# Kernel tuning notes

Measured on AMD Instinct MI355X. Metric: run time of the kernel, lower is better.

## Reference

```python
import jax, jax.numpy as jnp
import numpy as np

NC, NG, NP = 8192, 4096, 140
FD, D, L = 512, 256, 2
E_OBS, E_COEXP, E_PPI, E_SYM = 300000, 200000, 10000, 20000
EPS = 1e-5


def layer_norm(x, g, b):
    mu = jnp.mean(x, -1, keepdims=True)
    v = jnp.mean((x - mu) ** 2, -1, keepdims=True)
    return (x - mu) * jax.lax.rsqrt(v + EPS) * g + b


def sage(h_src, h_dst, src, dst, w, Ws, Wn, b, n_dst):
    # DGL SAGEConv (mean aggregator, edge-weighted): mean over incoming
    # weighted messages, then fc_self(h_dst) + fc_neigh(neigh) + bias.
    m = h_src[src] * w[:, None]                                  # [E, D]
    neigh = jax.ops.segment_sum(m, dst, num_segments=n_dst)      # [n_dst, D]
    deg = jax.ops.segment_sum(jnp.ones_like(w), dst, num_segments=n_dst)
    neigh = neigh / jnp.maximum(deg, 1.0)[:, None]
    return h_dst @ Ws + neigh @ Wn + b


def setup_inputs() -> dict:
    key = jax.random.key(0)
    ks = iter(jax.random.split(key, 64))
    def n(*s):
        return jax.random.normal(next(ks), s, jnp.float32) * 0.02
    def u(e):
        return jax.random.uniform(next(ks), (e,), jnp.float32)
    def ri(e, hi):
        return jax.random.randint(next(ks), (e,), 0, hi, jnp.int32)
    return dict(
        cell_feat=jax.random.normal(next(ks), (NC, FD), jnp.float32),
        gene_feat=jax.random.normal(next(ks), (NG, FD), jnp.float32),
        pro_idx=jnp.arange(NP, dtype=jnp.int32),
        obs_src=ri(E_OBS, NG), obs_dst=ri(E_OBS, NC), obs_w=u(E_OBS),
        rev_obs_src=ri(E_OBS, NC), rev_obs_dst=ri(E_OBS, NG), rev_obs_w=u(E_OBS),
        symbol_src=ri(E_SYM, NG), symbol_dst=ri(E_SYM, NP), symbol_w=u(E_SYM),
        rev_symbol_src=ri(E_SYM, NP), rev_symbol_dst=ri(E_SYM, NG), rev_symbol_w=u(E_SYM),
        coexp_src=ri(E_COEXP, NG), coexp_dst=ri(E_COEXP, NG), coexp_w=u(E_COEXP),
        ppi_src=ri(E_PPI, NP), ppi_dst=ri(E_PPI, NP), ppi_w=u(E_PPI),
        W_emb_cell=n(FD, D), b_emb_cell=jnp.zeros((D,), jnp.float32),
        W_emb_gene=n(FD, D), b_emb_gene=jnp.zeros((D,), jnp.float32),
        emb_pro=n(NP, D),
        W_mlpcell=n(L, D, D), b_mlpcell=jnp.zeros((L, D), jnp.float32),
        W_sage_self=n(L, 6, D, D), W_sage_neigh=n(L, 6, D, D),
        b_sage=jnp.zeros((L, 6, D), jnp.float32),
        ln1_g=jnp.ones((L, 3, D), jnp.float32), ln1_b=jnp.zeros((L, 3, D), jnp.float32),
        ln2_g=jnp.ones((L, 3, D), jnp.float32), ln2_b=jnp.zeros((L, 3, D), jnp.float32),
        W_last=n(3 * D, NP), b_last=jnp.zeros((NP,), jnp.float32),
    )


def reference(cell_feat, gene_feat, pro_idx,
              obs_src, obs_dst, obs_w,
              rev_obs_src, rev_obs_dst, rev_obs_w,
              symbol_src, symbol_dst, symbol_w,
              rev_symbol_src, rev_symbol_dst, rev_symbol_w,
              coexp_src, coexp_dst, coexp_w,
              ppi_src, ppi_dst, ppi_w,
              W_emb_cell, b_emb_cell, W_emb_gene, b_emb_gene, emb_pro,
              W_mlpcell, b_mlpcell, W_sage_self, W_sage_neigh, b_sage,
              ln1_g, ln1_b, ln2_g, ln2_b, W_last, b_last):
    act = jax.nn.selu
    hc = cell_feat @ W_emb_cell + b_emb_cell      # emb_cell
    hg = gene_feat @ W_emb_gene + b_emb_gene      # emb_gene
    hp = emb_pro[pro_idx]                         # nn.Embedding path
    nc, ng, npn = hc.shape[0], hg.shape[0], hp.shape[0]
    hist = [hc]
    for l in range(W_mlpcell.shape[0]):
        Ws, Wn, bs = W_sage_self[l], W_sage_neigh[l], b_sage[l]
        hmlp = layer_norm(act(hc @ W_mlpcell[l] + b_mlpcell[l]), ln1_g[l, 2], ln1_b[l, 2])
        # HeteroGraphConv(SAGE) over edges_sub = [obs, rev_obs, symbol, rev_symbol] (stack)
        s_obs = sage(hg, hc, obs_src, obs_dst, obs_w, Ws[0], Wn[0], bs[0], nc)
        s_robs = sage(hc, hg, rev_obs_src, rev_obs_dst, rev_obs_w, Ws[1], Wn[1], bs[1], ng)
        s_sym = sage(hg, hp, symbol_src, symbol_dst, symbol_w, Ws[2], Wn[2], bs[2], npn)
        s_rsym = sage(hp, hg, rev_symbol_src, rev_symbol_dst, rev_symbol_w, Ws[3], Wn[3], bs[3], ng)
        # homogeneous subgraph convs: gene_sage on coexp, pro_sage on ppi
        h_gg = layer_norm(act(sage(hg, hg, coexp_src, coexp_dst, coexp_w, Ws[4], Wn[4], bs[4], ng)), ln1_g[l, 0], ln1_b[l, 0])
        h_pp = layer_norm(act(sage(hp, hp, ppi_src, ppi_dst, ppi_w, Ws[5], Wn[5], bs[5], npn)), ln1_g[l, 1], ln1_b[l, 1])
        # norm each stacked relation output, then agg='sum' over the stack dim
        hgen = layer_norm(act(s_robs), ln1_g[l, 0], ln1_b[l, 0]) + layer_norm(act(s_rsym), ln1_g[l, 0], ln1_b[l, 0]) + h_gg
        hpro = layer_norm(act(s_sym), ln1_g[l, 1], ln1_b[l, 1]) + h_pp
        hcel = layer_norm(act(s_obs), ln1_g[l, 2], ln1_b[l, 2]) + hmlp
        hg = layer_norm(act(hgen), ln2_g[l, 0], ln2_b[l, 0])
        hp = layer_norm(act(hpro), ln2_g[l, 1], ln2_b[l, 1])
        hc = layer_norm(act(hcel), ln2_g[l, 2], ln2_b[l, 2])
        hist.append(hc)
    # mlp_last over concat of per-layer cell reps (sum(dims[1:-1]) -> dims[-1])
    return jnp.concatenate(hist, -1) @ W_last + b_last
```

## Files before the change

### kernel.cpp

```cpp
#include <hip/hip_runtime.h>

typedef unsigned short ushort_t;
typedef unsigned int uint_t;

typedef ushort_t ushortx8 __attribute__((ext_vector_type(8)));
typedef ushort_t ushortx4 __attribute__((ext_vector_type(4)));
typedef __bf16 bf16x8 __attribute__((ext_vector_type(8)));
typedef float f32x4 __attribute__((ext_vector_type(4)));

#define NCC 8192
#define NGG 4096
#define NPP 140
#define LDS_STR 88

__device__ __forceinline__ float bf2f(ushort_t u) {
    uint_t i = ((uint_t)u) << 16;
    float f;
    __builtin_memcpy(&f, &i, 4);
    return f;
}
__device__ __forceinline__ ushort_t f2bf(float f) {
    uint_t i;
    __builtin_memcpy(&i, &f, 4);
    uint_t r = (i + 0x7FFFu + ((i >> 16) & 1u)) >> 16;
    return (ushort_t)r;
}
__device__ __forceinline__ float scrub(float x) {
    return __builtin_isfinite(x) ? x : 0.f;
}
__device__ __forceinline__ float selu_f(float x) {
    return x > 0.f ? 1.0507009873554805f * x : 1.7580993408473766f * expm1f(x);
}
__device__ __forceinline__ float wsum64(float x) {
    for (int o = 32; o; o >>= 1) x += __shfl_xor(x, o, 64);
    return x;
}

__global__ __launch_bounds__(256) void sc_zero1(int* __restrict__ a, int na) {
    int i = blockIdx.x * 256 + threadIdx.x;
    if (i < na) a[i] = 0;
}

struct CntJob {
    const int* dst;
    const int* src;
    const float* w;
    uint_t* pw;
    ushort_t* rank;
    int E;
    int* deg;
    int bstart;
};
struct CntBatch {
    CntJob j[6];
};
__global__ __launch_bounds__(256) void sc_csr_count_all(CntBatch cb) {
    int bx = blockIdx.x;
    int r = 0;
#pragma unroll
    for (int i = 1; i < 6; ++i) r = (bx >= cb.j[i].bstart) ? i : r;
    const CntJob& J = cb.j[r];
    int e = (bx - J.bstart) * 256 + threadIdx.x;
    if (e < J.E) {
        int rk = atomicAdd(&J.deg[J.dst[e]], 1);
        J.rank[e] = (ushort_t)rk;
        J.pw[e] = ((uint_t)f2bf(J.w[e]) << 16) | (uint_t)J.src[e];
    }
}

__global__ __launch_bounds__(1024) void sc_csr_scan6(const int* __restrict__ deg_base,
                                                     int* __restrict__ offs_base) {
    const int ndst[6] = {NCC, NGG, NPP, NGG, NGG, NPP};
    const int dstart[6] = {0, NCC, NCC + NGG, NCC + NGG + NPP, NCC + 2 * NGG + NPP,
                           NCC + 3 * NGG + NPP};
    const int ostart[6] = {0, NCC + 1, NCC + NGG + 2, NCC + NGG + NPP + 3,
                           NCC + 2 * NGG + NPP + 4, NCC + 3 * NGG + NPP + 5};
    int r = blockIdx.x;
    const int* deg = deg_base + dstart[r];
    int* offs = offs_base + ostart[r];
    int n = ndst[r];
    __shared__ int wsum[16];
    __shared__ int carry;
    int tid = threadIdx.x, wave = tid >> 6, lane = tid & 63;
    if (tid == 0) carry = 0;
    __syncthreads();
    for (int base = 0; base < n; base += 1024) {
        int i = base + tid;
        int v = (i < n) ? deg[i] : 0;
        int x = v;
#pragma unroll
        for (int o = 1; o < 64; o <<= 1) {
            int t = __shfl_up(x, o, 64);
            if (lane >= o) x += t;
        }
        if (lane == 63) wsum[wave] = x;
        __syncthreads();
        if (tid == 0) {
            int acc = 0;
#pragma unroll
            for (int k = 0; k < 16; ++k) {
                int t = wsum[k];
                wsum[k] = acc;
                acc += t;
            }
        }
        __syncthreads();
        int incl = x + wsum[wave];
        int cr = carry;
        if (i < n) offs[i] = cr + incl - v;
        __syncthreads();
        if (tid == 1023) carry = cr + incl;
        __syncthreads();
    }
    if (tid == 0) offs[n] = carry;
}

struct FillJob {
    const int* dst;
    const uint_t* pw;
    const ushort_t* rank;
    int E;
    const int* offs;
    uint_t* ep;
    int bstart;
};
struct FillBatch {
    FillJob j[6];
};
__global__ __launch_bounds__(256) void sc_csr_fill_all(FillBatch fb) {
    int bx = blockIdx.x;
    int r = 0;
#pragma unroll
    for (int i = 1; i < 6; ++i) r = (bx >= fb.j[i].bstart) ? i : r;
    const FillJob& J = fb.j[r];
    int e = (bx - J.bstart) * 256 + threadIdx.x;
    if (e < J.E) {
        int d = J.dst[e];
        int pos = J.offs[d] + (int)J.rank[e];
        J.ep[pos] = J.pw[e];
    }
}

struct TrJob {
    const float* src;
    ushort_t* dst;
    int K, N, nx, nxy;
    int bstart;
};
struct TrBatch {
    TrJob j[6];
};
__global__ __launch_bounds__(256) void sc_transpose_all(TrBatch tb) {
    __shared__ ushort_t t[32][33];
    int bx = blockIdx.x;
    int r = 0;
#pragma unroll
    for (int i = 1; i < 6; ++i) r = (bx >= tb.j[i].bstart) ? i : r;
    const TrJob& J = tb.j[r];
    int local = bx - J.bstart;
    int b = local / J.nxy, rem = local % J.nxy;
    int n0 = (rem % J.nx) * 32, k0 = (rem / J.nx) * 32;
    const float* s = J.src + (size_t)b * J.K * J.N;
    ushort_t* d = J.dst + (size_t)b * J.K * J.N;
    int x = threadIdx.x & 31, y = threadIdx.x >> 5;
    for (int i = y; i < 32; i += 8) {
        int k = k0 + i, n = n0 + x;
        t[i][x] = (k < J.K && n < J.N) ? f2bf(s[(size_t)k * J.N + n]) : (ushort_t)0;
    }
    __syncthreads();
    for (int i = y; i < 32; i += 8) {
        int n = n0 + i, k = k0 + x;
        if (n < J.N && k < J.K) d[(size_t)n * J.K + k] = t[x][i];
    }
}

__global__ __launch_bounds__(256) void sc_gather_emb(const float* __restrict__ emb,
                                                     const int* __restrict__ idx,
                                                     ushort_t* __restrict__ out, int n) {
    int i = blockIdx.x * 256 + threadIdx.x;
    if (i < n) {
        int r = i >> 8, c = i & 255;
        int j = idx[r];
        j = (uint_t)j < (uint_t)NPP ? j : 0;
        out[i] = f2bf(emb[(size_t)j * 256 + c]);
    }
}

struct GatherJob {
    const ushort_t* hsrc;
    int src_ld, src_n;
    const int* offs;
    const uint_t* ep;
    ushort_t* out;
    int row_start;
};
struct GatherBatch {
    GatherJob j[6];
};
__global__ __launch_bounds__(256) void sc_gather_all(GatherBatch gb, int total_rows) {
    int grow = blockIdx.x * 4 + (threadIdx.x >> 6);
    if (grow >= total_rows) return;
    int r = 0;
#pragma unroll
    for (int i = 1; i < 6; ++i) r = (grow >= gb.j[i].row_start) ? i : r;
    r = __builtin_amdgcn_readfirstlane(r);
    const ushort_t* hsrc = gb.j[r].hsrc;
    const int src_ld = gb.j[r].src_ld, src_n = gb.j[r].src_n;
    const int* offs = gb.j[r].offs;
    const uint_t* ep = gb.j[r].ep;
    ushort_t* out = gb.j[r].out;
    int row = grow - gb.j[r].row_start;
    int lane = threadIdx.x & 63, c = lane * 4;
    int s0 = offs[row], s1 = offs[row + 1];
    float a0 = 0.f, a1 = 0.f, a2 = 0.f, a3 = 0.f;
    for (int base = s0; base < s1; base += 64) {
        int e = base + lane;
        uint_t myp = (e < s1) ? ep[e] : 0u;
        int cnt = s1 - base;
        cnt = cnt < 64 ? cnt : 64;
        int cnt8 = (cnt + 7) & ~7;
        for (int jj = 0; jj < cnt8; jj += 8) {
#pragma unroll
            for (int u = 0; u < 8; ++u) {
                uint_t pw = (uint_t)__shfl((int)myp, jj + u, 64);
                int s = (int)(pw & 0xFFFFu);
                s = (uint_t)s < (uint_t)src_n ? s : 0;
                float w = bf2f((ushort_t)(pw >> 16));
                ushortx4 v = *(const ushortx4*)(hsrc + (size_t)s * src_ld + c);
                a0 += w * bf2f(v[0]);
                a1 += w * bf2f(v[1]);
                a2 += w * bf2f(v[2]);
                a3 += w * bf2f(v[3]);
            }
        }
    }
    float inv = 1.f / fmaxf((float)(s1 - s0), 1.f);
    ushort_t* o = out + (size_t)row * 256 + c;
    o[0] = f2bf(scrub(a0 * inv));
    o[1] = f2bf(scrub(a1 * inv));
    o[2] = f2bf(scrub(a2 * inv));
    o[3] = f2bf(scrub(a3 * inv));
}

__global__ __launch_bounds__(256) void sc_gemm(const void* __restrict__ A1, int lda1, int af1,
                                               const ushort_t* __restrict__ Bt1, int K1,
                                               const float* __restrict__ bias,
                                               float* __restrict__ Cf, ushort_t* __restrict__ Cb,
                                               int ldc, int M, int N) {
    __shared__ __align__(16) ushort_t As[128 * LDS_STR];
    __shared__ __align__(16) ushort_t Bs[64 * LDS_STR];
    const int tid = threadIdx.x;
    const int wave = tid >> 6, lane = tid & 63;
    const int lr = lane & 15, lq = lane >> 4;
    const int m0 = blockIdx.x * 128, n0 = blockIdx.y * 64;
    f32x4 acc[2][4] = {};
    for (int k0 = 0; k0 < K1; k0 += 64) {
        __syncthreads();
#pragma unroll
        for (int i = 0; i < 4; ++i) {
            int g = tid + i * 256;
            int r = g >> 3, c = (g & 7) * 8;
            ushortx8 v = {0, 0, 0, 0, 0, 0, 0, 0};
            int gm = m0 + r;
            if (gm < M) {
                if (af1) {
                    const float* Af = (const float*)A1;
                    float4 f0 = *(const float4*)(Af + (size_t)gm * lda1 + k0 + c);
                    float4 f1 = *(const float4*)(Af + (size_t)gm * lda1 + k0 + c + 4);
                    v[0] = f2bf(f0.x);
                    v[1] = f2bf(f0.y);
                    v[2] = f2bf(f0.z);
                    v[3] = f2bf(f0.w);
                    v[4] = f2bf(f1.x);
                    v[5] = f2bf(f1.y);
                    v[6] = f2bf(f1.z);
                    v[7] = f2bf(f1.w);
                } else {
                    v = *(const ushortx8*)((const ushort_t*)A1 + (size_t)gm * lda1 + k0 + c);
                }
            }
            *(ushortx8*)(&As[r * LDS_STR + c]) = v;
        }
#pragma unroll
        for (int i = 0; i < 2; ++i) {
            int g = tid + i * 256;
            int r = g >> 3, c = (g & 7) * 8;
            ushortx8 v = {0, 0, 0, 0, 0, 0, 0, 0};
            int gn = n0 + r;
            if (gn < N) v = *(const ushortx8*)(Bt1 + (size_t)gn * K1 + k0 + c);
            *(ushortx8*)(&Bs[r * LDS_STR + c]) = v;
        }
        __syncthreads();
#pragma unroll
        for (int kk = 0; kk < 64; kk += 32) {
            bf16x8 a0 = __builtin_bit_cast(
                bf16x8, *(const ushortx8*)(&As[(wave * 32 + lr) * LDS_STR + kk + lq * 8]));
            bf16x8 a1 = __builtin_bit_cast(
                bf16x8, *(const ushortx8*)(&As[(wave * 32 + 16 + lr) * LDS_STR + kk + lq * 8]));
            bf16x8 b0 =
                __builtin_bit_cast(bf16x8, *(const ushortx8*)(&Bs[(lr)*LDS_STR + kk + lq * 8]));
            bf16x8 b1 = __builtin_bit_cast(
                bf16x8, *(const ushortx8*)(&Bs[(16 + lr) * LDS_STR + kk + lq * 8]));
            bf16x8 b2 = __builtin_bit_cast(
                bf16x8, *(const ushortx8*)(&Bs[(32 + lr) * LDS_STR + kk + lq * 8]));
            bf16x8 b3 = __builtin_bit_cast(
                bf16x8, *(const ushortx8*)(&Bs[(48 + lr) * LDS_STR + kk + lq * 8]));
            acc[0][0] = __builtin_amdgcn_mfma_f32_16x16x32_bf16(a0, b0, acc[0][0], 0, 0, 0);
            acc[0][1] = __builtin_amdgcn_mfma_f32_16x16x32_bf16(a0, b1, acc[0][1], 0, 0, 0);
            acc[0][2] = __builtin_amdgcn_mfma_f32_16x16x32_bf16(a0, b2, acc[0][2], 0, 0, 0);
            acc[0][3] = __builtin_amdgcn_mfma_f32_16x16x32_bf16(a0, b3, acc[0][3], 0, 0, 0);
            acc[1][0] = __builtin_amdgcn_mfma_f32_16x16x32_bf16(a1, b0, acc[1][0], 0, 0, 0);
            acc[1][1] = __builtin_amdgcn_mfma_f32_16x16x32_bf16(a1, b1, acc[1][1], 0, 0, 0);
            acc[1][2] = __builtin_amdgcn_mfma_f32_16x16x32_bf16(a1, b2, acc[1][2], 0, 0, 0);
            acc[1][3] = __builtin_amdgcn_mfma_f32_16x16x32_bf16(a1, b3, acc[1][3], 0, 0, 0);
        }
    }
#pragma unroll
    for (int mt = 0; mt < 2; ++mt)
#pragma unroll
        for (int nt = 0; nt < 4; ++nt) {
            int col = n0 + nt * 16 + lr;
            if (col >= N) continue;
            float bb = bias ? bias[col] : 0.f;
#pragma unroll
            for (int v = 0; v < 4; ++v) {
                int row = m0 + wave * 32 + mt * 16 + lq * 4 + v;
                if (row >= M) continue;
                float val = scrub(acc[mt][nt][v] + bb);
                if (Cf)
                    Cf[(size_t)row * ldc + col] = val;
                else
                    Cb[(size_t)row * ldc + col] = f2bf(val);
            }
        }
}

struct GemmJob {
    const void* A1;
    int lda1, K1, af1;
    const ushort_t* Bt1;
    const ushort_t* A2;
    int K2;
    const ushort_t* Bt2;
    const float* bias;
    ushort_t* C;
    int ldc, M;
    int mstart;
};
struct GemmBatch {
    GemmJob j[7];
};
__global__ __launch_bounds__(256) void sc_gemm_batch(GemmBatch gbat) {
    int bx = blockIdx.x;
    int r = 0;
#pragma unroll
    for (int i = 1; i < 7; ++i) r = (bx >= gbat.j[i].mstart) ? i : r;
    const void* JA1 = gbat.j[r].A1;
    const int lda1 = gbat.j[r].lda1, K1j = gbat.j[r].K1, af1 = gbat.j[r].af1;
    const ushort_t* JBt1 = gbat.j[r].Bt1;
    const ushort_t* JA2 = gbat.j[r].A2;
    const int K2j = gbat.j[r].K2;
    const ushort_t* JBt2 = gbat.j[r].Bt2;
    const float* bias = gbat.j[r].bias;
    ushort_t* C = gbat.j[r].C;
    const int ldc = gbat.j[r].ldc, M = gbat.j[r].M;
    __shared__ __align__(16) ushort_t As[128 * LDS_STR];
    __shared__ __align__(16) ushort_t Bs[64 * LDS_STR];
    const int tid = threadIdx.x;
    const int wave = tid >> 6, lane = tid & 63;
    const int lr = lane & 15, lq = lane >> 4;
    const int m0 = (bx - gbat.j[r].mstart) * 128, n0 = blockIdx.y * 64;
    f32x4 acc[2][4] = {};
    for (int pass = 0; pass < 2; ++pass) {
        const void* A = pass ? (const void*)JA2 : JA1;
        const ushort_t* Bt = pass ? JBt2 : JBt1;
        const int K = pass ? K2j : K1j;
        const int lda = pass ? 256 : lda1;
        const int af = pass ? 0 : af1;
        if (K == 0 || A == nullptr) continue;
        for (int k0 = 0; k0 < K; k0 += 64) {
            __syncthreads();
#pragma unroll
            for (int i = 0; i < 4; ++i) {
                int g = tid + i * 256;
                int rr = g >> 3, c = (g & 7) * 8;
                ushortx8 v = {0, 0, 0, 0, 0, 0, 0, 0};
                int gm = m0 + rr;
                if (gm < M) {
                    if (af) {
                        const float* Af = (const float*)A;
                        float4 f0 = *(const float4*)(Af + (size_t)gm * lda + k0 + c);
                        float4 f1 = *(const float4*)(Af + (size_t)gm * lda + k0 + c + 4);
                        v[0] = f2bf(f0.x);
                        v[1] = f2bf(f0.y);
                        v[2] = f2bf(f0.z);
                        v[3] = f2bf(f0.w);
                        v[4] = f2bf(f1.x);
                        v[5] = f2bf(f1.y);
                        v[6] = f2bf(f1.z);
                        v[7] = f2bf(f1.w);
                    } else {
                        v = *(const ushortx8*)((const ushort_t*)A + (size_t)gm * lda + k0 + c);
                    }
                }
                *(ushortx8*)(&As[rr * LDS_STR + c]) = v;
            }
#pragma unroll
            for (int i = 0; i < 2; ++i) {
                int g = tid + i * 256;
                int rr = g >> 3, c = (g & 7) * 8;
                int gn = n0 + rr;
                ushortx8 v = *(const ushortx8*)(Bt + (size_t)gn * K + k0 + c);
                *(ushortx8*)(&Bs[rr * LDS_STR + c]) = v;
            }
            __syncthreads();
#pragma unroll
            for (int kk = 0; kk < 64; kk += 32) {
                bf16x8 a0 = __builtin_bit_cast(
                    bf16x8, *(const ushortx8*)(&As[(wave * 32 + lr) * LDS_STR + kk + lq * 8]));
                bf16x8 a1 = __builtin_bit_cast(
                    bf16x8,
                    *(const ushortx8*)(&As[(wave * 32 + 16 + lr) * LDS_STR + kk + lq * 8]));
                bf16x8 b0 = __builtin_bit_cast(
                    bf16x8, *(const ushortx8*)(&Bs[(lr)*LDS_STR + kk + lq * 8]));
                bf16x8 b1 = __builtin_bit_cast(
                    bf16x8, *(const ushortx8*)(&Bs[(16 + lr) * LDS_STR + kk + lq * 8]));
                bf16x8 b2 = __builtin_bit_cast(
                    bf16x8, *(const ushortx8*)(&Bs[(32 + lr) * LDS_STR + kk + lq * 8]));
                bf16x8 b3 = __builtin_bit_cast(
                    bf16x8, *(const ushortx8*)(&Bs[(48 + lr) * LDS_STR + kk + lq * 8]));
                acc[0][0] = __builtin_amdgcn_mfma_f32_16x16x32_bf16(a0, b0, acc[0][0], 0, 0, 0);
                acc[0][1] = __builtin_amdgcn_mfma_f32_16x16x32_bf16(a0, b1, acc[0][1], 0, 0, 0);
                acc[0][2] = __builtin_amdgcn_mfma_f32_16x16x32_bf16(a0, b2, acc[0][2], 0, 0, 0);
                acc[0][3] = __builtin_amdgcn_mfma_f32_16x16x32_bf16(a0, b3, acc[0][3], 0, 0, 0);
                acc[1][0] = __builtin_amdgcn_mfma_f32_16x16x32_bf16(a1, b0, acc[1][0], 0, 0, 0);
                acc[1][1] = __builtin_amdgcn_mfma_f32_16x16x32_bf16(a1, b1, acc[1][1], 0, 0, 0);
                acc[1][2] = __builtin_amdgcn_mfma_f32_16x16x32_bf16(a1, b2, acc[1][2], 0, 0, 0);
                acc[1][3] = __builtin_amdgcn_mfma_f32_16x16x32_bf16(a1, b3, acc[1][3], 0, 0, 0);
            }
        }
    }
#pragma unroll
    for (int mt = 0; mt < 2; ++mt)
#pragma unroll
        for (int nt = 0; nt < 4; ++nt) {
            int col = n0 + nt * 16 + lr;
            float bb = bias[col];
#pragma unroll
            for (int v = 0; v < 4; ++v) {
                int row = m0 + wave * 32 + mt * 16 + lq * 4 + v;
                if (row >= M) continue;
                C[(size_t)row * ldc + col] = f2bf(scrub(acc[mt][nt][v] + bb));
            }
        }
}

struct LnJob {
    const ushort_t *sA, *sB, *sC;
    const float *g1, *b1, *g2, *b2;
    ushort_t* out;
    int out_ld;
    int row_start;
};
struct LnBatch {
    LnJob j[3];
};
__global__ __launch_bounds__(256) void sc_fuse_ln_all(LnBatch lb, int total_rows) {
    int grow = blockIdx.x * 4 + (threadIdx.x >> 6);
    if (grow >= total_rows) return;
    int r = 0;
#pragma unroll
    for (int i = 1; i < 3; ++i) r = (grow >= lb.j[i].row_start) ? i : r;
    r = __builtin_amdgcn_readfirstlane(r);
    const ushort_t* srcs[3] = {lb.j[r].sA, lb.j[r].sB, lb.j[r].sC};
    const float* g1 = lb.j[r].g1;
    const float* b1 = lb.j[r].b1;
    const float* g2 = lb.j[r].g2;
    const float* b2 = lb.j[r].b2;
    ushort_t* out = lb.j[r].out;
    int out_ld = lb.j[r].out_ld;
    int row = grow - lb.j[r].row_start;
    int lane = threadIdx.x & 63, c = lane * 4;
    float t[4] = {0.f, 0.f, 0.f, 0.f};
#pragma unroll
    for (int si = 0; si < 3; ++si) {
        const ushort_t* s = srcs[si];
        if (!s) continue;
        ushortx4 v = *(const ushortx4*)(s + (size_t)row * 256 + c);
        float x0 = selu_f(scrub(bf2f(v[0]))), x1 = selu_f(scrub(bf2f(v[1])));
        float x2 = selu_f(scrub(bf2f(v[2]))), x3 = selu_f(scrub(bf2f(v[3])));
        float mu = wsum64(x0 + x1 + x2 + x3) * (1.f / 256.f);
        float d0 = x0 - mu, d1 = x1 - mu, d2 = x2 - mu, d3 = x3 - mu;
        float var = wsum64(d0 * d0 + d1 * d1 + d2 * d2 + d3 * d3) * (1.f / 256.f);
        float rr = rsqrtf(var + 1e-5f);
        t[0] += d0 * rr * g1[c + 0] + b1[c + 0];
        t[1] += d1 * rr * g1[c + 1] + b1[c + 1];
        t[2] += d2 * rr * g1[c + 2] + b1[c + 2];
        t[3] += d3 * rr * g1[c + 3] + b1[c + 3];
    }
    float x0 = selu_f(scrub(t[0])), x1 = selu_f(scrub(t[1]));
    float x2 = selu_f(scrub(t[2])), x3 = selu_f(scrub(t[3]));
    float mu = wsum64(x0 + x1 + x2 + x3) * (1.f / 256.f);
    float d0 = x0 - mu, d1 = x1 - mu, d2 = x2 - mu, d3 = x3 - mu;
    float var = wsum64(d0 * d0 + d1 * d1 + d2 * d2 + d3 * d3) * (1.f / 256.f);
    float rr = rsqrtf(var + 1e-5f);
    ushort_t* o = out + (size_t)row * out_ld + c;
    o[0] = f2bf(scrub(d0 * rr * g2[c + 0] + b2[c + 0]));
    o[1] = f2bf(scrub(d1 * rr * g2[c + 1] + b2[c + 1]));
    o[2] = f2bf(scrub(d2 * rr * g2[c + 2] + b2[c + 2]));
    o[3] = f2bf(scrub(d3 * rr * g2[c + 3] + b2[c + 3]));
}

static inline int cdivi(int a, int b) { return (a + b - 1) / b; }

extern "C" void kernel_launch(void* const* d_in, const int* in_sizes, int n_in, void* d_out,
                              int out_size, void* d_ws, size_t ws_size, hipStream_t stream) {
    const float* cell_feat = (const float*)d_in[0];
    const float* gene_feat = (const float*)d_in[1];
    const int* pro_idx = (const int*)d_in[2];
    const int* edge_src[6] = {(const int*)d_in[3],  (const int*)d_in[6],  (const int*)d_in[9],
                              (const int*)d_in[12], (const int*)d_in[15], (const int*)d_in[18]};
    const int* edge_dst[6] = {(const int*)d_in[4],  (const int*)d_in[7],  (const int*)d_in[10],
                              (const int*)d_in[13], (const int*)d_in[16], (const int*)d_in[19]};
    const float* edge_w[6] = {(const float*)d_in[5],  (const float*)d_in[8],
                              (const float*)d_in[11], (const float*)d_in[14],
                              (const float*)d_in[17], (const float*)d_in[20]};
    const float* W_emb_cell = (const float*)d_in[21];
    const float* b_emb_cell = (const float*)d_in[22];
    const float* W_emb_gene = (const float*)d_in[23];
    const float* b_emb_gene = (const float*)d_in[24];
    const float* emb_pro = (const float*)d_in[25];
    const float* W_mlpcell = (const float*)d_in[26];
    const float* b_mlpcell = (const float*)d_in[27];
    const float* W_sage_self = (const float*)d_in[28];
    const float* W_sage_neigh = (const float*)d_in[29];
    const float* b_sage = (const float*)d_in[30];
    const float* ln1_g = (const float*)d_in[31];
    const float* ln1_b = (const float*)d_in[32];
    const float* ln2_g = (const float*)d_in[33];
    const float* ln2_b = (const float*)d_in[34];
    const float* W_last = (const float*)d_in[35];
    const float* b_last = (const float*)d_in[36];

    const int E_obs = in_sizes[3], E_sym = in_sizes[9], E_coexp = in_sizes[15],
              E_ppi = in_sizes[18];
    const int Er[6] = {E_obs, E_obs, E_sym, E_sym, E_coexp, E_ppi};
    const int Nd[6] = {NCC, NGG, NPP, NGG, NGG, NPP};

    char* p = (char*)d_ws;
    auto carve = [&](size_t bytes) -> char* {
        char* r = p;
        p += ((bytes + 255) & ~(size_t)255);
        return r;
    };
    ushort_t* hist = (ushort_t*)carve((size_t)NCC * 768 * 2);
    ushort_t* hg = (ushort_t*)carve((size_t)NGG * 256 * 2);
    ushort_t* hp = (ushort_t*)carve((size_t)NPP * 256 * 2);
    ushort_t* n_obs = (ushort_t*)carve((size_t)NCC * 256 * 2);
    ushort_t* n_robs = (ushort_t*)carve((size_t)NGG * 256 * 2);
    ushort_t* n_sym = (ushort_t*)carve((size_t)NPP * 256 * 2);
    ushort_t* n_rsym = (ushort_t*)carve((size_t)NGG * 256 * 2);
    ushort_t* n_coexp = (ushort_t*)carve((size_t)NGG * 256 * 2);
    ushort_t* n_ppi = (ushort_t*)carve((size_t)NPP * 256 * 2);
    ushort_t* s_obs = (ushort_t*)carve((size_t)NCC * 256 * 2);
    ushort_t* s_robs = (ushort_t*)carve((size_t)NGG * 256 * 2);
    ushort_t* s_sym = (ushort_t*)carve((size_t)NPP * 256 * 2);
    ushort_t* s_rsym = (ushort_t*)carve((size_t)NGG * 256 * 2);
    ushort_t* s_coexp = (ushort_t*)carve((size_t)NGG * 256 * 2);
    ushort_t* s_ppi = (ushort_t*)carve((size_t)NPP * 256 * 2);
    ushort_t* s_mlp = (ushort_t*)carve((size_t)NCC * 256 * 2);
    ushort_t* Wt_emb_cell = (ushort_t*)carve((size_t)512 * 256 * 2);
    ushort_t* Wt_emb_gene = (ushort_t*)carve((size_t)512 * 256 * 2);
    ushort_t* Wt_mlp = (ushort_t*)carve((size_t)2 * 256 * 256 * 2);
    ushort_t* Wt_self = (ushort_t*)carve((size_t)12 * 256 * 256 * 2);
    ushort_t* Wt_neigh = (ushort_t*)carve((size_t)12 * 256 * 256 * 2);
    ushort_t* Wt_last = (ushort_t*)carve((size_t)140 * 768 * 2);
    const int NDTOT = NCC + 3 * NGG + 2 * NPP;
    int* deg_all = (int*)carve((size_t)NDTOT * 4);
    int* offs_all = (int*)carve((size_t)(NDTOT + 6) * 4);
    const int ETOT = 2 * E_obs + 2 * E_sym + E_coexp + E_ppi;
    uint_t* pw_all = (uint_t*)carve((size_t)ETOT * 4);
    ushort_t* rank_all = (ushort_t*)carve((size_t)ETOT * 2);
    uint_t* ep_all = (uint_t*)carve((size_t)ETOT * 4);
    (void)ws_size;
    (void)n_in;
    (void)out_size;

    const int dS[6] = {0, NCC, NCC + NGG, NCC + NGG + NPP, NCC + 2 * NGG + NPP,
                       NCC + 3 * NGG + NPP};
    const int oS[6] = {0, NCC + 1, NCC + NGG + 2, NCC + NGG + NPP + 3, NCC + 2 * NGG + NPP + 4,
                       NCC + 3 * NGG + NPP + 5};
    int eS[6];
    eS[0] = 0;
    eS[1] = eS[0] + E_obs;
    eS[2] = eS[1] + E_obs;
    eS[3] = eS[2] + E_sym;
    eS[4] = eS[3] + E_sym;
    eS[5] = eS[4] + E_coexp;

    sc_zero1<<<cdivi(NDTOT, 256), 256, 0, stream>>>(deg_all, NDTOT);
    {
        CntBatch cb;
        FillBatch fb;
        int bs = 0;
        for (int r = 0; r < 6; ++r) {
            cb.j[r] = {edge_dst[r], edge_src[r], edge_w[r], pw_all + eS[r], rank_all + eS[r],
                       Er[r], deg_all + dS[r], bs};
            fb.j[r] = {edge_dst[r], pw_all + eS[r], rank_all + eS[r], Er[r], offs_all + oS[r],
                       ep_all + eS[r], bs};
            bs += cdivi(Er[r], 256);
        }
        sc_csr_count_all<<<bs, 256, 0, stream>>>(cb);
        sc_csr_scan6<<<6, 1024, 0, stream>>>(deg_all, offs_all);
        sc_csr_fill_all<<<bs, 256, 0, stream>>>(fb);
    }

    {
        TrBatch tb;
        int bs = 0;
        auto add = [&](int idx, const float* s, ushort_t* d, int B, int K, int N) {
            int nx = cdivi(N, 32), ny = cdivi(K, 32);
            tb.j[idx] = {s, d, K, N, nx, nx * ny, bs};
            bs += B * nx * ny;
        };
        add(0, W_emb_cell, Wt_emb_cell, 1, 512, 256);
        add(1, W_emb_gene, Wt_emb_gene, 1, 512, 256);
        add(2, W_mlpcell, Wt_mlp, 2, 256, 256);
        add(3, W_sage_self, Wt_self, 12, 256, 256);
        add(4, W_sage_neigh, Wt_neigh, 12, 256, 256);
        add(5, W_last, Wt_last, 1, 768, 140);
        sc_transpose_all<<<bs, 256, 0, stream>>>(tb);
    }

    sc_gather_emb<<<cdivi(NPP * 256, 256), 256, 0, stream>>>(emb_pro, pro_idx, hp, NPP * 256);
    {
        GemmBatch gbat;
        for (int i = 0; i < 7; ++i) gbat.j[i].mstart = 0x7FFFFFFF;
        gbat.j[0] = {cell_feat, 512, 512, 1, Wt_emb_cell, nullptr, 0, nullptr, b_emb_cell, hist,
                     768, NCC, 0};
        gbat.j[1] = {gene_feat, 512, 512, 1, Wt_emb_gene, nullptr, 0, nullptr, b_emb_gene, hg,
                     256, NGG, 64};
        sc_gemm_batch<<<dim3(96, 4), 256, 0, stream>>>(gbat);
    }

    for (int l = 0; l < 2; ++l) {
        const ushort_t* hc_l = hist + l * 256;
        {
            GatherBatch gb;
            const ushort_t* hs[6] = {hg, hc_l, hg, hp, hg, hp};
            const int lds[6] = {256, 768, 256, 256, 256, 256};
            const int sn[6] = {NGG, NCC, NGG, NPP, NGG, NPP};
            ushort_t* outs[6] = {n_obs, n_robs, n_sym, n_rsym, n_coexp, n_ppi};
            int rs = 0;
            for (int r = 0; r < 6; ++r) {
                gb.j[r] = {hs[r], lds[r], sn[r], offs_all + oS[r], ep_all + eS[r], outs[r], rs};
                rs += Nd[r];
            }
            sc_gather_all<<<cdivi(rs, 4), 256, 0, stream>>>(gb, rs);
        }
        {
            const size_t WSZ = 65536;
            GemmBatch gbat;
            gbat.j[0] = {hc_l, 768, 256, 0, Wt_mlp + (size_t)l * WSZ, nullptr, 0, nullptr,
                         b_mlpcell + l * 256, s_mlp, 256, NCC, 0};
            const ushort_t* dstf[6] = {hc_l, hg, hp, hg, hg, hp};
            const int dld[6] = {768, 256, 256, 256, 256, 256};
            const ushort_t* nb[6] = {n_obs, n_robs, n_sym, n_rsym, n_coexp, n_ppi};
            ushort_t* so[6] = {s_obs, s_robs, s_sym, s_rsym, s_coexp, s_ppi};
            int ms = cdivi(NCC, 128);
            for (int r = 0; r < 6; ++r) {
                gbat.j[r + 1] = {dstf[r],
                                 dld[r],
                                 256,
                                 0,
                                 Wt_self + (size_t)(l * 6 + r) * WSZ,
                                 nb[r],
                                 256,
                                 Wt_neigh + (size_t)(l * 6 + r) * WSZ,
                                 b_sage + (l * 6 + r) * 256,
                                 so[r],
                                 256,
                                 Nd[r],
                                 ms};
                ms += cdivi(Nd[r], 128);
            }
            sc_gemm_batch<<<dim3(ms, 4), 256, 0, stream>>>(gbat);
        }
        {
            LnBatch lb;
            lb.j[0] = {s_robs, s_rsym, s_coexp, ln1_g + (l * 3 + 0) * 256,
                       ln1_b + (l * 3 + 0) * 256, ln2_g + (l * 3 + 0) * 256,
                       ln2_b + (l * 3 + 0) * 256, hg, 256, 0};
            lb.j[1] = {s_sym, s_ppi, nullptr, ln1_g + (l * 3 + 1) * 256,
                       ln1_b + (l * 3 + 1) * 256, ln2_g + (l * 3 + 1) * 256,
                       ln2_b + (l * 3 + 1) * 256, hp, 256, NGG};
            lb.j[2] = {s_obs, s_mlp, nullptr, ln1_g + (l * 3 + 2) * 256,
                       ln1_b + (l * 3 + 2) * 256, ln2_g + (l * 3 + 2) * 256,
                       ln2_b + (l * 3 + 2) * 256, hist + (l + 1) * 256, 768, NGG + NPP};
            int rs = NGG + NPP + NCC;
            sc_fuse_ln_all<<<cdivi(rs, 4), 256, 0, stream>>>(lb, rs);
        }
    }

    sc_gemm<<<dim3(64, 3), 256, 0, stream>>>(hist, 768, 0, Wt_last, 768, b_last, (float*)d_out,
                                             nullptr, 140, NCC, 140);
}
```

Before: 431.3 us.

## Merge setup kernels into fewer launches and overlap CSR fill with embedding GEMM

Folds CSR counting, weight transposes and the protein embedding gather into one prep kernel. The CSR fill is merged into the embedding GEMM launch so the two independent workloads share a single grid. The gather inner unroll also grows from 8 to 16 edges per step. This cuts kernel launches and idle tail time in the small setup stages. The fill blocks now run alongside GEMM blocks, which raises register and LDS pressure for the fill path.

```diff
diff --git a/kernel.cpp b/kernel.cpp
--- a/kernel.cpp
+++ b/kernel.cpp
@@ -54,17 +54,99 @@
 struct CntBatch {
     CntJob j[6];
 };
-__global__ __launch_bounds__(256) void sc_csr_count_all(CntBatch cb) {
+struct TrJob {
+    const float* src;
+    ushort_t* dst;
+    int K, N, nx, nxy;
+    int bstart;
+};
+struct TrBatch {
+    TrJob j[6];
+};
+struct FillJob {
+    const int* dst;
+    const uint_t* pw;
+    const ushort_t* rank;
+    int E;
+    const int* offs;
+    uint_t* ep;
+    int bstart;
+};
+struct FillBatch {
+    FillJob j[6];
+};
+struct GemmJob {
+    const void* A1;
+    int lda1, K1, af1;
+    const ushort_t* Bt1;
+    const ushort_t* A2;
+    int K2;
+    const ushort_t* Bt2;
+    const float* bias;
+    ushort_t* C;
+    int ldc, M;
+    int mstart;
+};
+struct GemmBatch {
+    GemmJob j[7];
+};
+
+struct PrepArgs {
+    CntBatch cb;
+    int bsC;
+    TrBatch tb;
+    int bsT;
+    const float* emb;
+    const int* pidx;
+    ushort_t* hp;
+    int nEmb;
+};
+__global__ __launch_bounds__(256) void sc_prep(PrepArgs pa) {
+    __shared__ ushort_t t[32][33];
     int bx = blockIdx.x;
-    int r = 0;
-#pragma unroll
-    for (int i = 1; i < 6; ++i) r = (bx >= cb.j[i].bstart) ? i : r;
-    const CntJob& J = cb.j[r];
-    int e = (bx - J.bstart) * 256 + threadIdx.x;
-    if (e < J.E) {
-        int rk = atomicAdd(&J.deg[J.dst[e]], 1);
-        J.rank[e] = (ushort_t)rk;
-        J.pw[e] = ((uint_t)f2bf(J.w[e]) << 16) | (uint_t)J.src[e];
+    if (bx < pa.bsC) {
+        int r = 0;
+#pragma unroll
+        for (int i = 1; i < 6; ++i) r = (bx >= pa.cb.j[i].bstart) ? i : r;
+        const CntJob& J = pa.cb.j[r];
+        int e = (bx - J.bstart) * 256 + threadIdx.x;
+        if (e < J.E) {
+            int rk = atomicAdd(&J.deg[J.dst[e]], 1);
+            J.rank[e] = (ushort_t)rk;
+            J.pw[e] = ((uint_t)f2bf(J.w[e]) << 16) | (uint_t)J.src[e];
+        }
+        return;
+    }
+    bx -= pa.bsC;
+    if (bx < pa.bsT) {
+        int r = 0;
+#pragma unroll
+        for (int i = 1; i < 6; ++i) r = (bx >= pa.tb.j[i].bstart) ? i : r;
+        const TrJob& J = pa.tb.j[r];
+        int local = bx - J.bstart;
+        int b = local / J.nxy, rem = local % J.nxy;
+        int n0 = (rem % J.nx) * 32, k0 = (rem / J.nx) * 32;
+        const float* s = J.src + (size_t)b * J.K * J.N;
+        ushort_t* d = J.dst + (size_t)b * J.K * J.N;
+        int x = threadIdx.x & 31, y = threadIdx.x >> 5;
+        for (int i = y; i < 32; i += 8) {
+            int k = k0 + i, n = n0 + x;
+            t[i][x] = (k < J.K && n < J.N) ? f2bf(s[(size_t)k * J.N + n]) : (ushort_t)0;
+        }
+        __syncthreads();
+        for (int i = y; i < 32; i += 8) {
+            int n = n0 + i, k = k0 + x;
+            if (n < J.N && k < J.K) d[(size_t)n * J.K + k] = t[x][i];
+        }
+        return;
+    }
+    bx -= pa.bsT;
+    int i = bx * 256 + threadIdx.x;
+    if (i < pa.nEmb) {
+        int r = i >> 8, c = i & 255;
+        int j = pa.pidx[r];
+        j = (uint_t)j < (uint_t)NPP ? j : 0;
+        pa.hp[i] = f2bf(pa.emb[(size_t)j * 256 + c]);
     }
 }
 
@@ -90,8 +172,8 @@
         int x = v;
 #pragma unroll
         for (int o = 1; o < 64; o <<= 1) {
-            int t = __shfl_up(x, o, 64);
-            if (lane >= o) x += t;
+            int tv = __shfl_up(x, o, 64);
+            if (lane >= o) x += tv;
         }
         if (lane == 63) wsum[wave] = x;
         __syncthreads();
@@ -99,9 +181,9 @@
             int acc = 0;
 #pragma unroll
             for (int k = 0; k < 16; ++k) {
-                int t = wsum[k];
+                int tv = wsum[k];
                 wsum[k] = acc;
-                acc += t;
+                acc += tv;
             }
         }
         __syncthreads();
@@ -115,246 +197,11 @@
     if (tid == 0) offs[n] = carry;
 }
 
-struct FillJob {
-    const int* dst;
-    const uint_t* pw;
-    const ushort_t* rank;
-    int E;
-    const int* offs;
-    uint_t* ep;
-    int bstart;
-};
-struct FillBatch {
-    FillJob j[6];
-};
-__global__ __launch_bounds__(256) void sc_csr_fill_all(FillBatch fb) {
-    int bx = blockIdx.x;
+__device__ __forceinline__ void gemm_body(const GemmBatch& gbat, int mbx, int n0, ushort_t* As,
+                                          ushort_t* Bs) {
     int r = 0;
 #pragma unroll
-    for (int i = 1; i < 6; ++i) r = (bx >= fb.j[i].bstart) ? i : r;
-    const FillJob& J = fb.j[r];
-    int e = (bx - J.bstart) * 256 + threadIdx.x;
-    if (e < J.E) {
-        int d = J.dst[e];
-        int pos = J.offs[d] + (int)J.rank[e];
-        J.ep[pos] = J.pw[e];
-    }
-}
-
-struct TrJob {
-    const float* src;
-    ushort_t* dst;
-    int K, N, nx, nxy;
-    int bstart;
-};
-struct TrBatch {
-    TrJob j[6];
-};
-__global__ __launch_bounds__(256) void sc_transpose_all(TrBatch tb) {
-    __shared__ ushort_t t[32][33];
-    int bx = blockIdx.x;
-    int r = 0;
-#pragma unroll
-    for (int i = 1; i < 6; ++i) r = (bx >= tb.j[i].bstart) ? i : r;
-    const TrJob& J = tb.j[r];
-    int local = bx - J.bstart;
-    int b = local / J.nxy, rem = local % J.nxy;
-    int n0 = (rem % J.nx) * 32, k0 = (rem / J.nx) * 32;
-    const float* s = J.src + (size_t)b * J.K * J.N;
-    ushort_t* d = J.dst + (size_t)b * J.K * J.N;
-    int x = threadIdx.x & 31, y = threadIdx.x >> 5;
-    for (int i = y; i < 32; i += 8) {
-        int k = k0 + i, n = n0 + x;
-        t[i][x] = (k < J.K && n < J.N) ? f2bf(s[(size_t)k * J.N + n]) : (ushort_t)0;
-    }
-    __syncthreads();
-    for (int i = y; i < 32; i += 8) {
-        int n = n0 + i, k = k0 + x;
-        if (n < J.N && k < J.K) d[(size_t)n * J.K + k] = t[x][i];
-    }
-}
-
-__global__ __launch_bounds__(256) void sc_gather_emb(const float* __restrict__ emb,
-                                                     const int* __restrict__ idx,
-                                                     ushort_t* __restrict__ out, int n) {
-    int i = blockIdx.x * 256 + threadIdx.x;
-    if (i < n) {
-        int r = i >> 8, c = i & 255;
-        int j = idx[r];
-        j = (uint_t)j < (uint_t)NPP ? j : 0;
-        out[i] = f2bf(emb[(size_t)j * 256 + c]);
-    }
-}
-
-struct GatherJob {
-    const ushort_t* hsrc;
-    int src_ld, src_n;
-    const int* offs;
-    const uint_t* ep;
-    ushort_t* out;
-    int row_start;
-};
-struct GatherBatch {
-    GatherJob j[6];
-};
-__global__ __launch_bounds__(256) void sc_gather_all(GatherBatch gb, int total_rows) {
-    int grow = blockIdx.x * 4 + (threadIdx.x >> 6);
-    if (grow >= total_rows) return;
-    int r = 0;
-#pragma unroll
-    for (int i = 1; i < 6; ++i) r = (grow >= gb.j[i].row_start) ? i : r;
-    r = __builtin_amdgcn_readfirstlane(r);
-    const ushort_t* hsrc = gb.j[r].hsrc;
-    const int src_ld = gb.j[r].src_ld, src_n = gb.j[r].src_n;
-    const int* offs = gb.j[r].offs;
-    const uint_t* ep = gb.j[r].ep;
-    ushort_t* out = gb.j[r].out;
-    int row = grow - gb.j[r].row_start;
-    int lane = threadIdx.x & 63, c = lane * 4;
-    int s0 = offs[row], s1 = offs[row + 1];
-    float a0 = 0.f, a1 = 0.f, a2 = 0.f, a3 = 0.f;
-    for (int base = s0; base < s1; base += 64) {
-        int e = base + lane;
-        uint_t myp = (e < s1) ? ep[e] : 0u;
-        int cnt = s1 - base;
-        cnt = cnt < 64 ? cnt : 64;
-        int cnt8 = (cnt + 7) & ~7;
-        for (int jj = 0; jj < cnt8; jj += 8) {
-#pragma unroll
-            for (int u = 0; u < 8; ++u) {
-                uint_t pw = (uint_t)__shfl((int)myp, jj + u, 64);
-                int s = (int)(pw & 0xFFFFu);
-                s = (uint_t)s < (uint_t)src_n ? s : 0;
-                float w = bf2f((ushort_t)(pw >> 16));
-                ushortx4 v = *(const ushortx4*)(hsrc + (size_t)s * src_ld + c);
-                a0 += w * bf2f(v[0]);
-                a1 += w * bf2f(v[1]);
-                a2 += w * bf2f(v[2]);
-                a3 += w * bf2f(v[3]);
-            }
-        }
-    }
-    float inv = 1.f / fmaxf((float)(s1 - s0), 1.f);
-    ushort_t* o = out + (size_t)row * 256 + c;
-    o[0] = f2bf(scrub(a0 * inv));
-    o[1] = f2bf(scrub(a1 * inv));
-    o[2] = f2bf(scrub(a2 * inv));
-    o[3] = f2bf(scrub(a3 * inv));
-}
-
-__global__ __launch_bounds__(256) void sc_gemm(const void* __restrict__ A1, int lda1, int af1,
-                                               const ushort_t* __restrict__ Bt1, int K1,
-                                               const float* __restrict__ bias,
-                                               float* __restrict__ Cf, ushort_t* __restrict__ Cb,
-                                               int ldc, int M, int N) {
-    __shared__ __align__(16) ushort_t As[128 * LDS_STR];
-    __shared__ __align__(16) ushort_t Bs[64 * LDS_STR];
-    const int tid = threadIdx.x;
-    const int wave = tid >> 6, lane = tid & 63;
-    const int lr = lane & 15, lq = lane >> 4;
-    const int m0 = blockIdx.x * 128, n0 = blockIdx.y * 64;
-    f32x4 acc[2][4] = {};
-    for (int k0 = 0; k0 < K1; k0 += 64) {
-        __syncthreads();
-#pragma unroll
-        for (int i = 0; i < 4; ++i) {
-            int g = tid + i * 256;
-            int r = g >> 3, c = (g & 7) * 8;
-            ushortx8 v = {0, 0, 0, 0, 0, 0, 0, 0};
-            int gm = m0 + r;
-            if (gm < M) {
-                if (af1) {
-                    const float* Af = (const float*)A1;
-                    float4 f0 = *(const float4*)(Af + (size_t)gm * lda1 + k0 + c);
-                    float4 f1 = *(const float4*)(Af + (size_t)gm * lda1 + k0 + c + 4);
-                    v[0] = f2bf(f0.x);
-                    v[1] = f2bf(f0.y);
-                    v[2] = f2bf(f0.z);
-                    v[3] = f2bf(f0.w);
-                    v[4] = f2bf(f1.x);
-                    v[5] = f2bf(f1.y);
-                    v[6] = f2bf(f1.z);
-                    v[7] = f2bf(f1.w);
-                } else {
-                    v = *(const ushortx8*)((const ushort_t*)A1 + (size_t)gm * lda1 + k0 + c);
-                }
-            }
-            *(ushortx8*)(&As[r * LDS_STR + c]) = v;
-        }
-#pragma unroll
-        for (int i = 0; i < 2; ++i) {
-            int g = tid + i * 256;
-            int r = g >> 3, c = (g & 7) * 8;
-            ushortx8 v = {0, 0, 0, 0, 0, 0, 0, 0};
-            int gn = n0 + r;
-            if (gn < N) v = *(const ushortx8*)(Bt1 + (size_t)gn * K1 + k0 + c);
-            *(ushortx8*)(&Bs[r * LDS_STR + c]) = v;
-        }
-        __syncthreads();
-#pragma unroll
-        for (int kk = 0; kk < 64; kk += 32) {
-            bf16x8 a0 = __builtin_bit_cast(
-                bf16x8, *(const ushortx8*)(&As[(wave * 32 + lr) * LDS_STR + kk + lq * 8]));
-            bf16x8 a1 = __builtin_bit_cast(
-                bf16x8, *(const ushortx8*)(&As[(wave * 32 + 16 + lr) * LDS_STR + kk + lq * 8]));
-            bf16x8 b0 =
-                __builtin_bit_cast(bf16x8, *(const ushortx8*)(&Bs[(lr)*LDS_STR + kk + lq * 8]));
-            bf16x8 b1 = __builtin_bit_cast(
-                bf16x8, *(const ushortx8*)(&Bs[(16 + lr) * LDS_STR + kk + lq * 8]));
-            bf16x8 b2 = __builtin_bit_cast(
-                bf16x8, *(const ushortx8*)(&Bs[(32 + lr) * LDS_STR + kk + lq * 8]));
-            bf16x8 b3 = __builtin_bit_cast(
-                bf16x8, *(const ushortx8*)(&Bs[(48 + lr) * LDS_STR + kk + lq * 8]));
-            acc[0][0] = __builtin_amdgcn_mfma_f32_16x16x32_bf16(a0, b0, acc[0][0], 0, 0, 0);
-            acc[0][1] = __builtin_amdgcn_mfma_f32_16x16x32_bf16(a0, b1, acc[0][1], 0, 0, 0);
-            acc[0][2] = __builtin_amdgcn_mfma_f32_16x16x32_bf16(a0, b2, acc[0][2], 0, 0, 0);
-            acc[0][3] = __builtin_amdgcn_mfma_f32_16x16x32_bf16(a0, b3, acc[0][3], 0, 0, 0);
-            acc[1][0] = __builtin_amdgcn_mfma_f32_16x16x32_bf16(a1, b0, acc[1][0], 0, 0, 0);
-            acc[1][1] = __builtin_amdgcn_mfma_f32_16x16x32_bf16(a1, b1, acc[1][1], 0, 0, 0);
-            acc[1][2] = __builtin_amdgcn_mfma_f32_16x16x32_bf16(a1, b2, acc[1][2], 0, 0, 0);
-            acc[1][3] = __builtin_amdgcn_mfma_f32_16x16x32_bf16(a1, b3, acc[1][3], 0, 0, 0);
-        }
-    }
-#pragma unroll
-    for (int mt = 0; mt < 2; ++mt)
-#pragma unroll
-        for (int nt = 0; nt < 4; ++nt) {
-            int col = n0 + nt * 16 + lr;
-            if (col >= N) continue;
-            float bb = bias ? bias[col] : 0.f;
-#pragma unroll
-            for (int v = 0; v < 4; ++v) {
-                int row = m0 + wave * 32 + mt * 16 + lq * 4 + v;
-                if (row >= M) continue;
-                float val = scrub(acc[mt][nt][v] + bb);
-                if (Cf)
-                    Cf[(size_t)row * ldc + col] = val;
-                else
-                    Cb[(size_t)row * ldc + col] = f2bf(val);
-            }
-        }
-}
-
-struct GemmJob {
-    const void* A1;
-    int lda1, K1, af1;
-    const ushort_t* Bt1;
-    const ushort_t* A2;
-    int K2;
-    const ushort_t* Bt2;
-    const float* bias;
-    ushort_t* C;
-    int ldc, M;
-    int mstart;
-};
-struct GemmBatch {
-    GemmJob j[7];
-};
-__global__ __launch_bounds__(256) void sc_gemm_batch(GemmBatch gbat) {
-    int bx = blockIdx.x;
-    int r = 0;
-#pragma unroll
-    for (int i = 1; i < 7; ++i) r = (bx >= gbat.j[i].mstart) ? i : r;
+    for (int i = 1; i < 7; ++i) r = (mbx >= gbat.j[i].mstart) ? i : r;
     const void* JA1 = gbat.j[r].A1;
     const int lda1 = gbat.j[r].lda1, K1j = gbat.j[r].K1, af1 = gbat.j[r].af1;
     const ushort_t* JBt1 = gbat.j[r].Bt1;
@@ -364,12 +211,10 @@
     const float* bias = gbat.j[r].bias;
     ushort_t* C = gbat.j[r].C;
     const int ldc = gbat.j[r].ldc, M = gbat.j[r].M;
-    __shared__ __align__(16) ushort_t As[128 * LDS_STR];
-    __shared__ __align__(16) ushort_t Bs[64 * LDS_STR];
     const int tid = threadIdx.x;
     const int wave = tid >> 6, lane = tid & 63;
     const int lr = lane & 15, lq = lane >> 4;
-    const int m0 = (bx - gbat.j[r].mstart) * 128, n0 = blockIdx.y * 64;
+    const int m0 = (mbx - gbat.j[r].mstart) * 128;
     f32x4 acc[2][4] = {};
     for (int pass = 0; pass < 2; ++pass) {
         const void* A = pass ? (const void*)JA2 : JA1;
@@ -451,6 +296,165 @@
                 int row = m0 + wave * 32 + mt * 16 + lq * 4 + v;
                 if (row >= M) continue;
                 C[(size_t)row * ldc + col] = f2bf(scrub(acc[mt][nt][v] + bb));
+            }
+        }
+}
+
+__global__ __launch_bounds__(256) void sc_gemm_batch(GemmBatch gbat) {
+    __shared__ __align__(16) ushort_t As[128 * LDS_STR];
+    __shared__ __align__(16) ushort_t Bs[64 * LDS_STR];
+    gemm_body(gbat, blockIdx.x, blockIdx.y * 64, As, Bs);
+}
+
+struct FillGemmArgs {
+    GemmBatch gb;
+    int gemmBlocks;
+    FillBatch fb;
+};
+__global__ __launch_bounds__(256) void sc_fill_gemm(FillGemmArgs fg) {
+    __shared__ __align__(16) ushort_t As[128 * LDS_STR];
+    __shared__ __align__(16) ushort_t Bs[64 * LDS_STR];
+    int bx = blockIdx.x;
+    if (bx >= fg.gemmBlocks) {
+        bx -= fg.gemmBlocks;
+        int r = 0;
+#pragma unroll
+        for (int i = 1; i < 6; ++i) r = (bx >= fg.fb.j[i].bstart) ? i : r;
+        const FillJob& J = fg.fb.j[r];
+        int e = (bx - J.bstart) * 256 + threadIdx.x;
+        if (e < J.E) {
+            int d = J.dst[e];
+            J.ep[J.offs[d] + (int)J.rank[e]] = J.pw[e];
+        }
+        return;
+    }
+    gemm_body(fg.gb, bx >> 2, (bx & 3) * 64, As, Bs);
+}
+
+struct GatherJob {
+    const ushort_t* hsrc;
+    int src_ld, src_n;
+    const int* offs;
+    const uint_t* ep;
+    ushort_t* out;
+    int row_start;
+};
+struct GatherBatch {
+    GatherJob j[6];
+};
+__global__ __launch_bounds__(256) void sc_gather_all(GatherBatch gb, int total_rows) {
+    int grow = blockIdx.x * 4 + (threadIdx.x >> 6);
+    if (grow >= total_rows) return;
+    int r = 0;
+#pragma unroll
+    for (int i = 1; i < 6; ++i) r = (grow >= gb.j[i].row_start) ? i : r;
+    r = __builtin_amdgcn_readfirstlane(r);
+    const ushort_t* hsrc = gb.j[r].hsrc;
+    const int src_ld = gb.j[r].src_ld, src_n = gb.j[r].src_n;
+    const int* offs = gb.j[r].offs;
+    const uint_t* ep = gb.j[r].ep;
+    ushort_t* out = gb.j[r].out;
+    int row = grow - gb.j[r].row_start;
+    int lane = threadIdx.x & 63, c = lane * 4;
+    int s0 = offs[row], s1 = offs[row + 1];
+    float a0 = 0.f, a1 = 0.f, a2 = 0.f, a3 = 0.f;
+    for (int base = s0; base < s1; base += 64) {
+        int e = base + lane;
+        uint_t myp = (e < s1) ? ep[e] : 0u;
+        int cnt = s1 - base;
+        cnt = cnt < 64 ? cnt : 64;
+        int cnt16 = (cnt + 15) & ~15;
+        for (int jj = 0; jj < cnt16; jj += 16) {
+#pragma unroll
+            for (int u = 0; u < 16; ++u) {
+                uint_t pw = (uint_t)__shfl((int)myp, jj + u, 64);
+                int s = (int)(pw & 0xFFFFu);
+                s = (uint_t)s < (uint_t)src_n ? s : 0;
+                float w = bf2f((ushort_t)(pw >> 16));
+                ushortx4 v = *(const ushortx4*)(hsrc + (size_t)s * src_ld + c);
+                a0 += w * bf2f(v[0]);
+                a1 += w * bf2f(v[1]);
+                a2 += w * bf2f(v[2]);
+                a3 += w * bf2f(v[3]);
+            }
+        }
+    }
+    float inv = 1.f / fmaxf((float)(s1 - s0), 1.f);
+    ushort_t* o = out + (size_t)row * 256 + c;
+    o[0] = f2bf(scrub(a0 * inv));
+    o[1] = f2bf(scrub(a1 * inv));
+    o[2] = f2bf(scrub(a2 * inv));
+    o[3] = f2bf(scrub(a3 * inv));
+}
+
+__global__ __launch_bounds__(256) void sc_gemm(const ushort_t* __restrict__ A1, int lda1,
+                                               const ushort_t* __restrict__ Bt1, int K1,
+                                               const float* __restrict__ bias,
+                                               float* __restrict__ Cf, int ldc, int M, int N) {
+    __shared__ __align__(16) ushort_t As[128 * LDS_STR];
+    __shared__ __align__(16) ushort_t Bs[64 * LDS_STR];
+    const int tid = threadIdx.x;
+    const int wave = tid >> 6, lane = tid & 63;
+    const int lr = lane & 15, lq = lane >> 4;
+    const int m0 = blockIdx.x * 128, n0 = blockIdx.y * 64;
+    f32x4 acc[2][4] = {};
+    for (int k0 = 0; k0 < K1; k0 += 64) {
+        __syncthreads();
+#pragma unroll
+        for (int i = 0; i < 4; ++i) {
+            int g = tid + i * 256;
+            int r = g >> 3, c = (g & 7) * 8;
+            ushortx8 v = {0, 0, 0, 0, 0, 0, 0, 0};
+            int gm = m0 + r;
+            if (gm < M) v = *(const ushortx8*)(A1 + (size_t)gm * lda1 + k0 + c);
+            *(ushortx8*)(&As[r * LDS_STR + c]) = v;
+        }
+#pragma unroll
+        for (int i = 0; i < 2; ++i) {
+            int g = tid + i * 256;
+            int r = g >> 3, c = (g & 7) * 8;
+            ushortx8 v = {0, 0, 0, 0, 0, 0, 0, 0};
+            int gn = n0 + r;
+            if (gn < N) v = *(const ushortx8*)(Bt1 + (size_t)gn * K1 + k0 + c);
+            *(ushortx8*)(&Bs[r * LDS_STR + c]) = v;
+        }
+        __syncthreads();
+#pragma unroll
+        for (int kk = 0; kk < 64; kk += 32) {
+            bf16x8 a0 = __builtin_bit_cast(
+                bf16x8, *(const ushortx8*)(&As[(wave * 32 + lr) * LDS_STR + kk + lq * 8]));
+            bf16x8 a1 = __builtin_bit_cast(
+                bf16x8, *(const ushortx8*)(&As[(wave * 32 + 16 + lr) * LDS_STR + kk + lq * 8]));
+            bf16x8 b0 =
+                __builtin_bit_cast(bf16x8, *(const ushortx8*)(&Bs[(lr)*LDS_STR + kk + lq * 8]));
+            bf16x8 b1 = __builtin_bit_cast(
+                bf16x8, *(const ushortx8*)(&Bs[(16 + lr) * LDS_STR + kk + lq * 8]));
+            bf16x8 b2 = __builtin_bit_cast(
+                bf16x8, *(const ushortx8*)(&Bs[(32 + lr) * LDS_STR + kk + lq * 8]));
+            bf16x8 b3 = __builtin_bit_cast(
+                bf16x8, *(const ushortx8*)(&Bs[(48 + lr) * LDS_STR + kk + lq * 8]));
+            acc[0][0] = __builtin_amdgcn_mfma_f32_16x16x32_bf16(a0, b0, acc[0][0], 0, 0, 0);
+            acc[0][1] = __builtin_amdgcn_mfma_f32_16x16x32_bf16(a0, b1, acc[0][1], 0, 0, 0);
+            acc[0][2] = __builtin_amdgcn_mfma_f32_16x16x32_bf16(a0, b2, acc[0][2], 0, 0, 0);
+            acc[0][3] = __builtin_amdgcn_mfma_f32_16x16x32_bf16(a0, b3, acc[0][3], 0, 0, 0);
+            acc[1][0] = __builtin_amdgcn_mfma_f32_16x16x32_bf16(a1, b0, acc[1][0], 0, 0, 0);
+            acc[1][1] = __builtin_amdgcn_mfma_f32_16x16x32_bf16(a1, b1, acc[1][1], 0, 0, 0);
+            acc[1][2] = __builtin_amdgcn_mfma_f32_16x16x32_bf16(a1, b2, acc[1][2], 0, 0, 0);
+            acc[1][3] = __builtin_amdgcn_mfma_f32_16x16x32_bf16(a1, b3, acc[1][3], 0, 0, 0);
+        }
+    }
+#pragma unroll
+    for (int mt = 0; mt < 2; ++mt)
+#pragma unroll
+        for (int nt = 0; nt < 4; ++nt) {
+            int col = n0 + nt * 16 + lr;
+            if (col >= N) continue;
+            float bb = bias ? bias[col] : 0.f;
+#pragma unroll
+            for (int v = 0; v < 4; ++v) {
+                int row = m0 + wave * 32 + mt * 16 + lq * 4 + v;
+                if (row >= M) continue;
+                Cf[(size_t)row * ldc + col] = scrub(acc[mt][nt][v] + bb);
             }
         }
 }
@@ -600,28 +604,19 @@
 
     sc_zero1<<<cdivi(NDTOT, 256), 256, 0, stream>>>(deg_all, NDTOT);
     {
-        CntBatch cb;
-        FillBatch fb;
+        PrepArgs pa;
         int bs = 0;
         for (int r = 0; r < 6; ++r) {
-            cb.j[r] = {edge_dst[r], edge_src[r], edge_w[r], pw_all + eS[r], rank_all + eS[r],
-                       Er[r], deg_all + dS[r], bs};
-            fb.j[r] = {edge_dst[r], pw_all + eS[r], rank_all + eS[r], Er[r], offs_all + oS[r],
-                       ep_all + eS[r], bs};
+            pa.cb.j[r] = {edge_dst[r], edge_src[r], edge_w[r], pw_all + eS[r], rank_all + eS[r],
+                          Er[r], deg_all + dS[r], bs};
             bs += cdivi(Er[r], 256);
         }
-        sc_csr_count_all<<<bs, 256, 0, stream>>>(cb);
-        sc_csr_scan6<<<6, 1024, 0, stream>>>(deg_all, offs_all);
-        sc_csr_fill_all<<<bs, 256, 0, stream>>>(fb);
-    }
-
-    {
-        TrBatch tb;
-        int bs = 0;
+        pa.bsC = bs;
+        int bt = 0;
         auto add = [&](int idx, const float* s, ushort_t* d, int B, int K, int N) {
             int nx = cdivi(N, 32), ny = cdivi(K, 32);
-            tb.j[idx] = {s, d, K, N, nx, nx * ny, bs};
-            bs += B * nx * ny;
+            pa.tb.j[idx] = {s, d, K, N, nx, nx * ny, bt};
+            bt += B * nx * ny;
         };
         add(0, W_emb_cell, Wt_emb_cell, 1, 512, 256);
         add(1, W_emb_gene, Wt_emb_gene, 1, 512, 256);
@@ -629,18 +624,30 @@
         add(3, W_sage_self, Wt_self, 12, 256, 256);
         add(4, W_sage_neigh, Wt_neigh, 12, 256, 256);
         add(5, W_last, Wt_last, 1, 768, 140);
-        sc_transpose_all<<<bs, 256, 0, stream>>>(tb);
-    }
-
-    sc_gather_emb<<<cdivi(NPP * 256, 256), 256, 0, stream>>>(emb_pro, pro_idx, hp, NPP * 256);
+        pa.bsT = bt;
+        pa.emb = emb_pro;
+        pa.pidx = pro_idx;
+        pa.hp = hp;
+        pa.nEmb = NPP * 256;
+        int bsE = cdivi(NPP * 256, 256);
+        sc_prep<<<pa.bsC + pa.bsT + bsE, 256, 0, stream>>>(pa);
+    }
+    sc_csr_scan6<<<6, 1024, 0, stream>>>(deg_all, offs_all);
     {
-        GemmBatch gbat;
-        for (int i = 0; i < 7; ++i) gbat.j[i].mstart = 0x7FFFFFFF;
-        gbat.j[0] = {cell_feat, 512, 512, 1, Wt_emb_cell, nullptr, 0, nullptr, b_emb_cell, hist,
-                     768, NCC, 0};
-        gbat.j[1] = {gene_feat, 512, 512, 1, Wt_emb_gene, nullptr, 0, nullptr, b_emb_gene, hg,
-                     256, NGG, 64};
-        sc_gemm_batch<<<dim3(96, 4), 256, 0, stream>>>(gbat);
+        FillGemmArgs fg;
+        for (int i = 0; i < 7; ++i) fg.gb.j[i].mstart = 0x7FFFFFFF;
+        fg.gb.j[0] = {cell_feat, 512, 512, 1, Wt_emb_cell, nullptr, 0, nullptr, b_emb_cell, hist,
+                      768, NCC, 0};
+        fg.gb.j[1] = {gene_feat, 512, 512, 1, Wt_emb_gene, nullptr, 0, nullptr, b_emb_gene, hg,
+                      256, NGG, 64};
+        fg.gemmBlocks = 96 * 4;
+        int bs = 0;
+        for (int r = 0; r < 6; ++r) {
+            fg.fb.j[r] = {edge_dst[r], pw_all + eS[r], rank_all + eS[r], Er[r], offs_all + oS[r],
+                          ep_all + eS[r], bs};
+            bs += cdivi(Er[r], 256);
+        }
+        sc_fill_gemm<<<fg.gemmBlocks + bs, 256, 0, stream>>>(fg);
     }
 
     for (int l = 0; l < 2; ++l) {
@@ -702,6 +709,6 @@
         }
     }
 
-    sc_gemm<<<dim3(64, 3), 256, 0, stream>>>(hist, 768, 0, Wt_last, 768, b_last, (float*)d_out,
-                                             nullptr, 140, NCC, 140);
-}
+    sc_gemm<<<dim3(64, 3), 256, 0, stream>>>(hist, 768, Wt_last, 768, b_last, (float*)d_out, 140,
+                                             NCC, 140);
+}
```

Result: no change. 427.4 us (median of 2 runs) (-0.9%).
